# Kernel tuning notes

Measured on AMD Instinct MI355X. Metric: run time of the kernel, lower is better.

## Reference

```python
import jax, jax.numpy as jnp
import numpy as np

EPS = 1e-12  # torch F.normalize default eps
DN = ('NCHW', 'OIHW', 'NCHW')

def _conv(x, w, groups=1):
    return jax.lax.conv_general_dilated(x, w, window_strides=(1, 1), padding='SAME',
                                        feature_group_count=groups, dimension_numbers=DN)

def setup_inputs() -> dict:
    key = jax.random.key(0)
    k1, k2, k3, k4 = jax.random.split(key, 4)
    b, c, h, w = 4, 64, 64, 64
    x = jax.random.normal(k1, (b, c, h, w), dtype=jnp.float32)
    w_qkv = jax.random.normal(k2, (3 * c, c, 1, 1), dtype=jnp.float32) * (1.0 / np.sqrt(c))
    w_dw = jax.random.normal(k3, (3 * c, 1, 3, 3), dtype=jnp.float32) * (1.0 / 3.0)
    w_proj = jax.random.normal(k4, (c, c, 3, 3), dtype=jnp.float32) * (1.0 / np.sqrt(9 * c))
    return {"x": x, "w_qkv": w_qkv, "w_dw": w_dw, "w_proj": w_proj}

def _l2norm(t):
    # torch F.normalize(dim=-1): t / max(||t||_2, eps)
    n = jnp.sqrt(jnp.sum(t * t, axis=-1, keepdims=True))
    return t / jnp.maximum(n, EPS)

def reference(x, w_qkv, w_dw, w_proj):
    b, c, h, w = x.shape
    qkv = _conv(_conv(x, w_qkv), w_dw, groups=3 * c)  # (b, 3c, h, w)
    q, k, v = jnp.split(qkv, 3, axis=1)
    hw = h * w
    q = _l2norm(q.reshape(b, c, hw))  # normalize each channel's spatial vector
    k = _l2norm(k.reshape(b, c, hw))
    v = v.reshape(b, c, hw)
    attn = jnp.einsum('bcn,bcm->bnm', q, k)        # (b, hw, hw) cosine scores
    attn = jax.nn.softmax(attn, axis=-1)
    out = jnp.einsum('bcm,bmn->bcn', v, attn)       # v @ attn
    out = out.reshape(b, c, h, w)
    return _conv(out, w_proj)
```

## Files before the change

### kernel.cpp

```cpp
#include <hip/hip_runtime.h>
#include <hip/hip_bf16.h>

typedef __attribute__((ext_vector_type(8))) short bf16x8;
typedef __attribute__((ext_vector_type(4))) float f32x4;
typedef __attribute__((ext_vector_type(8))) unsigned short ushort8;

#define HW 4096
#define NC 64
#define PROWS 4356

static __device__ __forceinline__ unsigned short f2bf(float f) {
    unsigned int u = __float_as_uint(f);
    unsigned int r = (u + 0x7FFFu + ((u >> 16) & 1u)) >> 16;
    return (unsigned short)r;
}

__global__ __launch_bounds__(256) void k_conv1x1(const float* __restrict__ x,
                                                 const float* __restrict__ wqkv,
                                                 float* __restrict__ out) {
    __shared__ float wl[512];
    int nb = blockIdx.x, ocg = blockIdx.y, b = blockIdx.z;
    int t = threadIdx.x;
    for (int i = t; i < 512; i += 256) wl[i] = wqkv[ocg * 512 + i];
    __syncthreads();
    int n = nb * 256 + t;
    const float* xb = x + (size_t)b * NC * HW + n;
    float acc[8] = {0.f,0.f,0.f,0.f,0.f,0.f,0.f,0.f};
    for (int ic = 0; ic < 64; ic++) {
        float xv = xb[(size_t)ic * HW];
        #pragma unroll
        for (int o = 0; o < 8; o++) acc[o] += wl[o * 64 + ic] * xv;
    }
    float* ob = out + (size_t)b * 192 * HW + (size_t)(ocg * 8) * HW + n;
    #pragma unroll
    for (int o = 0; o < 8; o++) ob[(size_t)o * HW] = acc[o];
}

__global__ __launch_bounds__(256) void k_dwconv(const float* __restrict__ in,
                                                const float* __restrict__ wdw,
                                                float* __restrict__ out) {
    int yg = blockIdx.x, ch = blockIdx.y, b = blockIdx.z;
    int t = threadIdx.x;
    int y = yg * 4 + (t >> 6), xx = t & 63;
    const float* ib = in + ((size_t)b * 192 + ch) * HW;
    const float* wp = wdw + ch * 9;
    float s = 0.f;
    #pragma unroll
    for (int dy = 0; dy < 3; dy++) {
        int yy = y + dy - 1;
        if (yy < 0 || yy > 63) continue;
        const float* r = ib + yy * 64;
        float v0 = (xx > 0) ? r[xx - 1] : 0.f;
        float v1 = r[xx];
        float v2 = (xx < 63) ? r[xx + 1] : 0.f;
        const float* wr = wp + dy * 3;
        s += wr[0] * v0 + wr[1] * v1 + wr[2] * v2;
    }
    out[((size_t)b * 192 + ch) * HW + y * 64 + xx] = s;
}

__global__ __launch_bounds__(256) void k_norms(const float* __restrict__ qkv,
                                               float* __restrict__ invn) {
    int ch = blockIdx.x, b = blockIdx.y;
    const float* p = qkv + ((size_t)b * 192 + ch) * HW;
    float s = 0.f;
    for (int i = threadIdx.x; i < HW; i += 256) { float v = p[i]; s += v * v; }
    #pragma unroll
    for (int m = 1; m < 64; m <<= 1) s += __shfl_xor(s, m);
    __shared__ float red[4];
    if ((threadIdx.x & 63) == 0) red[threadIdx.x >> 6] = s;
    __syncthreads();
    if (threadIdx.x == 0) {
        float tot = red[0] + red[1] + red[2] + red[3];
        float nrm = sqrtf(tot);
        invn[b * 128 + ch] = 1.f / fmaxf(nrm, 1e-12f);
    }
}

__global__ __launch_bounds__(256) void k_pack(const float* __restrict__ qkv,
                                              const float* __restrict__ invn,
                                              unsigned short* __restrict__ qT,
                                              unsigned short* __restrict__ kT,
                                              unsigned short* __restrict__ vn) {
    int nb = blockIdx.x, sel = blockIdx.y, b = blockIdx.z;
    int n = nb * 256 + threadIdx.x;
    if (sel == 2) {
        const float* src = qkv + ((size_t)b * 192 + 128) * HW + n;
        unsigned short* dst = vn + (size_t)b * NC * HW + n;
        for (int c = 0; c < 64; c++) dst[(size_t)c * HW] = f2bf(src[(size_t)c * HW]);
    } else {
        const float* src = qkv + ((size_t)b * 192 + sel * 64) * HW + n;
        const float* iv = invn + b * 128 + sel * 64;
        unsigned short* dst = (sel == 0 ? qT : kT) + ((size_t)b * HW + n) * NC;
        for (int c0 = 0; c0 < 64; c0 += 8) {
            ushort8 pk;
            #pragma unroll
            for (int j = 0; j < 8; j++)
                pk[j] = f2bf(src[(size_t)(c0 + j) * HW] * iv[c0 + j]);
            *reinterpret_cast<ushort8*>(dst + c0) = pk;
        }
    }
}

__global__ __launch_bounds__(256) void k_rowsum(const unsigned short* __restrict__ qT,
                                                const unsigned short* __restrict__ kT,
                                                float* __restrict__ part) {
    __shared__ __align__(16) unsigned short klds[2][64 * 72];
    int mblk = blockIdx.x, ns = blockIdx.y, b = blockIdx.z;
    int t = threadIdx.x;
    int w = t >> 6, lane = t & 63, g = lane >> 4, r15 = lane & 15;
    const unsigned short* qb = qT + (size_t)b * HW * NC;
    const unsigned short* kb = kT + (size_t)b * HW * NC;
    int m0 = mblk * 128 + w * 16;
    const unsigned short* qp0 = qb + (size_t)(m0 + r15) * NC + g * 8;
    const unsigned short* qp1 = qb + (size_t)(m0 + 64 + r15) * NC + g * 8;
    bf16x8 a0 = *reinterpret_cast<const bf16x8*>(qp0);
    bf16x8 a1 = *reinterpret_cast<const bf16x8*>(qp0 + 32);
    bf16x8 a2 = *reinterpret_cast<const bf16x8*>(qp1);
    bf16x8 a3 = *reinterpret_cast<const bf16x8*>(qp1 + 32);
    float sa[4] = {0.f, 0.f, 0.f, 0.f};
    float sb[4] = {0.f, 0.f, 0.f, 0.f};
    int nbase = ns * 512;
    int nl = t >> 2, seg = t & 3;
    {
        const unsigned short* sp = kb + (size_t)(nbase + nl) * NC + seg * 16;
        *reinterpret_cast<ushort8*>(&klds[0][nl * 72 + seg * 16]) = *reinterpret_cast<const ushort8*>(sp);
        *reinterpret_cast<ushort8*>(&klds[0][nl * 72 + seg * 16 + 8]) = *reinterpret_cast<const ushort8*>(sp + 8);
    }
    __syncthreads();
    int cur = 0;
    for (int it = 0; it < 8; it++) {
        ushort8 r0, r1;
        bool hasnext = it < 7;
        if (hasnext) {
            const unsigned short* sp = kb + (size_t)(nbase + (it + 1) * 64 + nl) * NC + seg * 16;
            r0 = *reinterpret_cast<const ushort8*>(sp);
            r1 = *reinterpret_cast<const ushort8*>(sp + 8);
        }
        #pragma unroll
        for (int tt = 0; tt < 4; tt++) {
            const unsigned short* kp = &klds[cur][(tt * 16 + r15) * 72 + g * 8];
            bf16x8 b0 = *reinterpret_cast<const bf16x8*>(kp);
            bf16x8 b1 = *reinterpret_cast<const bf16x8*>(kp + 32);
            f32x4 d0 = {0.f, 0.f, 0.f, 0.f};
            f32x4 d1 = {0.f, 0.f, 0.f, 0.f};
            d0 = __builtin_amdgcn_mfma_f32_16x16x32_bf16(a0, b0, d0, 0, 0, 0);
            d1 = __builtin_amdgcn_mfma_f32_16x16x32_bf16(a2, b0, d1, 0, 0, 0);
            d0 = __builtin_amdgcn_mfma_f32_16x16x32_bf16(a1, b1, d0, 0, 0, 0);
            d1 = __builtin_amdgcn_mfma_f32_16x16x32_bf16(a3, b1, d1, 0, 0, 0);
            #pragma unroll
            for (int r = 0; r < 4; r++) { sa[r] += __expf(d0[r]); sb[r] += __expf(d1[r]); }
        }
        if (hasnext) {
            *reinterpret_cast<ushort8*>(&klds[cur ^ 1][nl * 72 + seg * 16]) = r0;
            *reinterpret_cast<ushort8*>(&klds[cur ^ 1][nl * 72 + seg * 16 + 8]) = r1;
            cur ^= 1;
        }
        __syncthreads();
    }
    #pragma unroll
    for (int off = 1; off < 16; off <<= 1) {
        #pragma unroll
        for (int r = 0; r < 4; r++) {
            sa[r] += __shfl_xor(sa[r], off);
            sb[r] += __shfl_xor(sb[r], off);
        }
    }
    if (r15 == 0) {
        size_t base = ((size_t)ns * 4 + b) * HW;
        f32x4 va = {sa[0], sa[1], sa[2], sa[3]};
        f32x4 vb = {sb[0], sb[1], sb[2], sb[3]};
        *reinterpret_cast<f32x4*>(&part[base + m0 + g * 4]) = va;
        *reinterpret_cast<f32x4*>(&part[base + m0 + 64 + g * 4]) = vb;
    }
}

__global__ __launch_bounds__(256) void k_recip(const float* __restrict__ part,
                                               float* __restrict__ inv) {
    int i = blockIdx.x * 256 + threadIdx.x;
    float s = 0.f;
    #pragma unroll
    for (int ns = 0; ns < 8; ns++) s += part[i + ns * 4 * HW];
    inv[i] = 1.f / s;
}

__global__ __launch_bounds__(512, 2) void k_attn_fused(const unsigned short* __restrict__ qT,
                                                       const unsigned short* __restrict__ kT,
                                                       const unsigned short* __restrict__ vn,
                                                       const float* __restrict__ rowinv,
                                                       unsigned short* __restrict__ inP) {
    __shared__ float red[8][64][8];
    int nb = blockIdx.x, b = blockIdx.y;
    int t = threadIdx.x;
    int w = t >> 6, lane = t & 63, g = lane >> 4, r15 = lane & 15;
    int n0 = nb * 64;
    const unsigned short* qb = qT + (size_t)b * HW * NC;
    const unsigned short* kbp = kT + (size_t)b * HW * NC;
    const unsigned short* vb = vn + (size_t)b * NC * HW;
    const float* rib = rowinv + (size_t)b * HW;
    bf16x8 kf0[4], kf1[4];
    #pragma unroll
    for (int tt = 0; tt < 4; tt++) {
        const unsigned short* kp = kbp + (size_t)(n0 + tt * 16 + r15) * NC + g * 8;
        kf0[tt] = *reinterpret_cast<const bf16x8*>(kp);
        kf1[tt] = *reinterpret_cast<const bf16x8*>(kp + 32);
    }
    f32x4 acc[4][4];
    #pragma unroll
    for (int ct = 0; ct < 4; ct++)
        #pragma unroll
        for (int tt = 0; tt < 4; tt++) acc[ct][tt] = f32x4{0.f, 0.f, 0.f, 0.f};
    int mw = w * 32;
    int qrow = (r15 >> 2) * 8 + (r15 & 3);
    const unsigned short* qrp = qb + (size_t)(mw + qrow) * NC;
    bf16x8 qa[2][2];
    #pragma unroll
    for (int ts = 0; ts < 2; ts++) {
        qa[ts][0] = *reinterpret_cast<const bf16x8*>(qrp + ts * 4 * NC + g * 8);
        qa[ts][1] = *reinterpret_cast<const bf16x8*>(qrp + ts * 4 * NC + 32 + g * 8);
    }
    f32x4 iv[2];
    iv[0] = *reinterpret_cast<const f32x4*>(rib + mw + g * 8);
    iv[1] = *reinterpret_cast<const f32x4*>(rib + mw + g * 8 + 4);
    for (int it = 0; it < 16; it++) {
        int mb = it * 256;
        bf16x8 va[4];
        #pragma unroll
        for (int ct = 0; ct < 4; ct++)
            va[ct] = *reinterpret_cast<const bf16x8*>(vb + (size_t)(ct * 16 + r15) * HW + mb + mw + g * 8);
        int adv = (it < 15) ? 256 : 0;
        const unsigned short* qrn = qrp + (size_t)adv * NC;
        bf16x8 qn[2][2];
        #pragma unroll
        for (int ts = 0; ts < 2; ts++) {
            qn[ts][0] = *reinterpret_cast<const bf16x8*>(qrn + ts * 4 * NC + g * 8);
            qn[ts][1] = *reinterpret_cast<const bf16x8*>(qrn + ts * 4 * NC + 32 + g * 8);
        }
        f32x4 ivn0 = *reinterpret_cast<const f32x4*>(rib + mb + adv + mw + g * 8);
        f32x4 ivn1 = *reinterpret_cast<const f32x4*>(rib + mb + adv + mw + g * 8 + 4);
        bf16x8 pb[4];
        #pragma unroll
        for (int tt = 0; tt < 4; tt++) {
            f32x4 z = {0.f, 0.f, 0.f, 0.f};
            f32x4 d0 = __builtin_amdgcn_mfma_f32_16x16x32_bf16(qa[0][0], kf0[tt], z, 0, 0, 0);
            d0 = __builtin_amdgcn_mfma_f32_16x16x32_bf16(qa[0][1], kf1[tt], d0, 0, 0, 0);
            f32x4 d1 = __builtin_amdgcn_mfma_f32_16x16x32_bf16(qa[1][0], kf0[tt], z, 0, 0, 0);
            d1 = __builtin_amdgcn_mfma_f32_16x16x32_bf16(qa[1][1], kf1[tt], d1, 0, 0, 0);
            float e0 = __expf(d0[0]) * iv[0][0];
            float e1 = __expf(d0[1]) * iv[0][1];
            float e2 = __expf(d0[2]) * iv[0][2];
            float e3 = __expf(d0[3]) * iv[0][3];
            float f0 = __expf(d1[0]) * iv[1][0];
            float f1 = __expf(d1[1]) * iv[1][1];
            float f2 = __expf(d1[2]) * iv[1][2];
            float f3 = __expf(d1[3]) * iv[1][3];
            unsigned int p0, p1, p2, p3;
            asm("v_cvt_pk_bf16_f32 %0, %1, %2" : "=v"(p0) : "v"(e0), "v"(e1));
            asm("v_cvt_pk_bf16_f32 %0, %1, %2" : "=v"(p1) : "v"(e2), "v"(e3));
            asm("v_cvt_pk_bf16_f32 %0, %1, %2" : "=v"(p2) : "v"(f0), "v"(f1));
            asm("v_cvt_pk_bf16_f32 %0, %1, %2" : "=v"(p3) : "v"(f2), "v"(f3));
            union { unsigned int u[4]; bf16x8 v; } pu;
            pu.u[0] = p0; pu.u[1] = p1; pu.u[2] = p2; pu.u[3] = p3;
            pb[tt] = pu.v;
        }
        #pragma unroll
        for (int ct = 0; ct < 4; ct++)
            #pragma unroll
            for (int tt = 0; tt < 4; tt++)
                acc[ct][tt] = __builtin_amdgcn_mfma_f32_16x16x32_bf16(va[ct], pb[tt], acc[ct][tt], 0, 0, 0);
        #pragma unroll
        for (int ts = 0; ts < 2; ts++) { qa[ts][0] = qn[ts][0]; qa[ts][1] = qn[ts][1]; }
        iv[0] = ivn0; iv[1] = ivn1;
        qrp += (size_t)adv * NC;
    }
    #pragma unroll
    for (int ph = 0; ph < 8; ph++) {
        int ct = ph >> 1, th = ph & 1;
        *reinterpret_cast<f32x4*>(&red[w][lane][0]) = acc[ct][th * 2];
        *reinterpret_cast<f32x4*>(&red[w][lane][4]) = acc[ct][th * 2 + 1];
        __syncthreads();
        int lr = t >> 3, kk = t & 7;
        float s = 0.f;
        #pragma unroll
        for (int ww = 0; ww < 8; ww++) s += red[ww][lr][kk];
        int c = ct * 16 + ((lr >> 4) << 2) + (kk & 3);
        int nn = n0 + (th * 2 + (kk >> 2)) * 16 + (lr & 15);
        int y = nn >> 6, xx = nn & 63;
        inP[((size_t)b * PROWS + (size_t)(y + 1) * 66 + 1 + xx) * 64 + c] = f2bf(s);
        __syncthreads();
    }
}

__global__ __launch_bounds__(256) void k_zero(float4* __restrict__ p, int n4) {
    int i = blockIdx.x * 256 + threadIdx.x;
    if (i < n4) p[i] = make_float4(0.f, 0.f, 0.f, 0.f);
}

__global__ __launch_bounds__(256) void k_wconv(const float* __restrict__ wp,
                                               unsigned short* __restrict__ wbf) {
    int idx = blockIdx.x * 256 + threadIdx.x;
    int tap = idx >> 12;
    int rem = idx & 4095;
    int oc = rem >> 6, ic = rem & 63;
    wbf[idx] = f2bf(wp[(oc * 64 + ic) * 9 + tap]);
}

__global__ __launch_bounds__(256) void k_proj_mfma(const unsigned short* __restrict__ inP,
                                                   const unsigned short* __restrict__ wbf,
                                                   float* __restrict__ out) {
    int nb = blockIdx.x, b = blockIdx.y;
    int t = threadIdx.x;
    int w = t >> 6, lane = t & 63, g = lane >> 4, r15 = lane & 15;
    int y = nb >> 1;
    int x0 = (nb & 1) * 32 + (w & 1) * 16;
    int oc0 = (w >> 1) * 32;
    const unsigned short* base = inP + (size_t)b * PROWS * 64;
    f32x4 acc[2] = {{0.f,0.f,0.f,0.f},{0.f,0.f,0.f,0.f}};
    #pragma unroll
    for (int tap = 0; tap < 9; tap++) {
        int dy = tap / 3, dx = tap % 3;
        int p = (y + dy) * 66 + x0 + dx + r15;
        const unsigned short* bp = base + (size_t)p * 64 + g * 8;
        bf16x8 b0 = *reinterpret_cast<const bf16x8*>(bp);
        bf16x8 b1 = *reinterpret_cast<const bf16x8*>(bp + 32);
        #pragma unroll
        for (int tt = 0; tt < 2; tt++) {
            const unsigned short* ap = wbf + tap * 4096 + (size_t)(oc0 + tt * 16 + r15) * 64 + g * 8;
            bf16x8 a0 = *reinterpret_cast<const bf16x8*>(ap);
            bf16x8 a1 = *reinterpret_cast<const bf16x8*>(ap + 32);
            acc[tt] = __builtin_amdgcn_mfma_f32_16x16x32_bf16(a0, b0, acc[tt], 0, 0, 0);
            acc[tt] = __builtin_amdgcn_mfma_f32_16x16x32_bf16(a1, b1, acc[tt], 0, 0, 0);
        }
    }
    int n0 = y * 64 + x0;
    #pragma unroll
    for (int tt = 0; tt < 2; tt++) {
        #pragma unroll
        for (int r = 0; r < 4; r++)
            out[((size_t)b * 64 + oc0 + tt * 16 + g * 4 + r) * HW + n0 + r15] = acc[tt][r];
    }
}

extern "C" void kernel_launch(void* const* d_in, const int* in_sizes, int n_in,
                              void* d_out, int out_size, void* d_ws, size_t ws_size,
                              hipStream_t stream) {
    const float* x    = (const float*)d_in[0];
    const float* wqkv = (const float*)d_in[1];
    const float* wdw  = (const float*)d_in[2];
    const float* wprj = (const float*)d_in[3];
    char* ws = (char*)d_ws;
    float* qkv_raw       = (float*)(ws + 0);
    float* qkv           = (float*)(ws + 12582912);
    unsigned short* qT   = (unsigned short*)(ws + 25165824);
    unsigned short* kT   = (unsigned short*)(ws + 27262976);
    unsigned short* vn   = (unsigned short*)(ws + 29360128);
    float* invn          = (float*)(ws + 31457280);
    float* rowsum_part   = (float*)(ws + 31459328);
    float* rowinv        = (float*)(ws + 31983616);
    unsigned short* wbf  = (unsigned short*)(ws + 32049152);
    unsigned short* inP  = (unsigned short*)(ws + 32122880);

    int inP4 = (4 * PROWS * 64 * 2) / 16;
    k_zero       <<<dim3((inP4 + 255) / 256), 256, 0, stream>>>((float4*)inP, inP4);
    k_wconv      <<<dim3(144),        256, 0, stream>>>(wprj, wbf);
    k_conv1x1    <<<dim3(16, 24, 4),  256, 0, stream>>>(x, wqkv, qkv_raw);
    k_dwconv     <<<dim3(16, 192, 4), 256, 0, stream>>>(qkv_raw, wdw, qkv);
    k_norms      <<<dim3(128, 4),     256, 0, stream>>>(qkv, invn);
    k_pack       <<<dim3(16, 3, 4),   256, 0, stream>>>(qkv, invn, qT, kT, vn);
    k_rowsum     <<<dim3(32, 8, 4),   256, 0, stream>>>(qT, kT, rowsum_part);
    k_recip      <<<dim3(64),         256, 0, stream>>>(rowsum_part, rowinv);
    k_attn_fused <<<dim3(64, 4),      512, 0, stream>>>(qT, kT, vn, rowinv, inP);
    k_proj_mfma  <<<dim3(128, 4),     256, 0, stream>>>(inP, wbf, (float*)d_out);
}
```

Baseline: 115.8 us.

## Fuse norms into dwconv, fold softmax scaling into exp2 and halve attention tile

The depthwise conv now emits partial sums of squares, and a tiny kernel folds both q and k inverse norms plus log2(e) into a single per-channel scale applied to k. This removes the separate norm reduction pass. The row-sum reciprocal becomes -log2(sum), which is injected as the MFMA accumulator init, so exp2 directly yields normalized probabilities and the per-element multiply disappears. The attention kernel's column tile is halved to 32 with launch bounds of 4 waves per SIMD, doubling the grid for occupancy. The cost is that each block reloads the q fragments without software prefetch, and bf16 rounding now applies to the combined scale.

Measured after the change: 146.4 us. 1.26x slower.

```diff
diff --git a/kernel.cpp b/kernel.cpp
--- a/kernel.cpp
+++ b/kernel.cpp
@@ -38,7 +38,8 @@
 
 __global__ __launch_bounds__(256) void k_dwconv(const float* __restrict__ in,
                                                 const float* __restrict__ wdw,
-                                                float* __restrict__ out) {
+                                                float* __restrict__ out,
+                                                float* __restrict__ psq) {
     int yg = blockIdx.x, ch = blockIdx.y, b = blockIdx.z;
     int t = threadIdx.x;
     int y = yg * 4 + (t >> 6), xx = t & 63;
@@ -57,28 +58,34 @@
         s += wr[0] * v0 + wr[1] * v1 + wr[2] * v2;
     }
     out[((size_t)b * 192 + ch) * HW + y * 64 + xx] = s;
-}
-
-__global__ __launch_bounds__(256) void k_norms(const float* __restrict__ qkv,
-                                               float* __restrict__ invn) {
-    int ch = blockIdx.x, b = blockIdx.y;
-    const float* p = qkv + ((size_t)b * 192 + ch) * HW;
-    float s = 0.f;
-    for (int i = threadIdx.x; i < HW; i += 256) { float v = p[i]; s += v * v; }
-    #pragma unroll
-    for (int m = 1; m < 64; m <<= 1) s += __shfl_xor(s, m);
-    __shared__ float red[4];
-    if ((threadIdx.x & 63) == 0) red[threadIdx.x >> 6] = s;
-    __syncthreads();
-    if (threadIdx.x == 0) {
-        float tot = red[0] + red[1] + red[2] + red[3];
-        float nrm = sqrtf(tot);
-        invn[b * 128 + ch] = 1.f / fmaxf(nrm, 1e-12f);
-    }
+    if (ch < 128) {
+        float sq = s * s;
+        #pragma unroll
+        for (int m = 1; m < 64; m <<= 1) sq += __shfl_xor(sq, m);
+        __shared__ float red[4];
+        if ((t & 63) == 0) red[t >> 6] = sq;
+        __syncthreads();
+        if (t == 0)
+            psq[((size_t)b * 128 + ch) * 16 + yg] = red[0] + red[1] + red[2] + red[3];
+    }
+}
+
+__global__ __launch_bounds__(256) void k_scales(const float* __restrict__ psq,
+                                                float* __restrict__ wk) {
+    int i = threadIdx.x;
+    int b = i >> 6, c = i & 63;
+    const float* pq = psq + ((size_t)b * 128 + c) * 16;
+    const float* pk = psq + ((size_t)b * 128 + 64 + c) * 16;
+    float sq = 0.f, sk = 0.f;
+    #pragma unroll
+    for (int j = 0; j < 16; j++) { sq += pq[j]; sk += pk[j]; }
+    float nq = fmaxf(sqrtf(sq), 1e-12f);
+    float nk = fmaxf(sqrtf(sk), 1e-12f);
+    wk[i] = 1.4426950408889634f / (nq * nk);
 }
 
 __global__ __launch_bounds__(256) void k_pack(const float* __restrict__ qkv,
-                                              const float* __restrict__ invn,
+                                              const float* __restrict__ wk,
                                               unsigned short* __restrict__ qT,
                                               unsigned short* __restrict__ kT,
                                               unsigned short* __restrict__ vn) {
@@ -88,15 +95,24 @@
         const float* src = qkv + ((size_t)b * 192 + 128) * HW + n;
         unsigned short* dst = vn + (size_t)b * NC * HW + n;
         for (int c = 0; c < 64; c++) dst[(size_t)c * HW] = f2bf(src[(size_t)c * HW]);
+    } else if (sel == 0) {
+        const float* src = qkv + (size_t)b * 192 * HW + n;
+        unsigned short* dst = qT + ((size_t)b * HW + n) * NC;
+        for (int c0 = 0; c0 < 64; c0 += 8) {
+            ushort8 pk;
+            #pragma unroll
+            for (int j = 0; j < 8; j++) pk[j] = f2bf(src[(size_t)(c0 + j) * HW]);
+            *reinterpret_cast<ushort8*>(dst + c0) = pk;
+        }
     } else {
-        const float* src = qkv + ((size_t)b * 192 + sel * 64) * HW + n;
-        const float* iv = invn + b * 128 + sel * 64;
-        unsigned short* dst = (sel == 0 ? qT : kT) + ((size_t)b * HW + n) * NC;
+        const float* src = qkv + ((size_t)b * 192 + 64) * HW + n;
+        const float* wv = wk + b * 64;
+        unsigned short* dst = kT + ((size_t)b * HW + n) * NC;
         for (int c0 = 0; c0 < 64; c0 += 8) {
             ushort8 pk;
             #pragma unroll
             for (int j = 0; j < 8; j++)
-                pk[j] = f2bf(src[(size_t)(c0 + j) * HW] * iv[c0 + j]);
+                pk[j] = f2bf(src[(size_t)(c0 + j) * HW] * wv[c0 + j]);
             *reinterpret_cast<ushort8*>(dst + c0) = pk;
         }
     }
@@ -149,7 +165,7 @@
             d0 = __builtin_amdgcn_mfma_f32_16x16x32_bf16(a1, b1, d0, 0, 0, 0);
             d1 = __builtin_amdgcn_mfma_f32_16x16x32_bf16(a3, b1, d1, 0, 0, 0);
             #pragma unroll
-            for (int r = 0; r < 4; r++) { sa[r] += __expf(d0[r]); sb[r] += __expf(d1[r]); }
+            for (int r = 0; r < 4; r++) { sa[r] += exp2f(d0[r]); sb[r] += exp2f(d1[r]); }
         }
         if (hasnext) {
             *reinterpret_cast<ushort8*>(&klds[cur ^ 1][nl * 72 + seg * 16]) = r0;
@@ -175,85 +191,71 @@
     }
 }
 
-__global__ __launch_bounds__(256) void k_recip(const float* __restrict__ part,
-                                               float* __restrict__ inv) {
+__global__ __launch_bounds__(256) void k_l2i(const float* __restrict__ part,
+                                             float* __restrict__ l2i) {
     int i = blockIdx.x * 256 + threadIdx.x;
     float s = 0.f;
     #pragma unroll
     for (int ns = 0; ns < 8; ns++) s += part[i + ns * 4 * HW];
-    inv[i] = 1.f / s;
-}
-
-__global__ __launch_bounds__(512, 2) void k_attn_fused(const unsigned short* __restrict__ qT,
+    l2i[i] = -log2f(s);
+}
+
+__global__ __launch_bounds__(512, 4) void k_attn_fused(const unsigned short* __restrict__ qT,
                                                        const unsigned short* __restrict__ kT,
                                                        const unsigned short* __restrict__ vn,
-                                                       const float* __restrict__ rowinv,
+                                                       const float* __restrict__ l2i,
                                                        unsigned short* __restrict__ inP) {
     __shared__ float red[8][64][8];
     int nb = blockIdx.x, b = blockIdx.y;
     int t = threadIdx.x;
     int w = t >> 6, lane = t & 63, g = lane >> 4, r15 = lane & 15;
-    int n0 = nb * 64;
+    int n0 = nb * 32;
     const unsigned short* qb = qT + (size_t)b * HW * NC;
     const unsigned short* kbp = kT + (size_t)b * HW * NC;
     const unsigned short* vb = vn + (size_t)b * NC * HW;
-    const float* rib = rowinv + (size_t)b * HW;
-    bf16x8 kf0[4], kf1[4];
-    #pragma unroll
-    for (int tt = 0; tt < 4; tt++) {
+    const float* rib = l2i + (size_t)b * HW;
+    bf16x8 kf0[2], kf1[2];
+    #pragma unroll
+    for (int tt = 0; tt < 2; tt++) {
         const unsigned short* kp = kbp + (size_t)(n0 + tt * 16 + r15) * NC + g * 8;
         kf0[tt] = *reinterpret_cast<const bf16x8*>(kp);
         kf1[tt] = *reinterpret_cast<const bf16x8*>(kp + 32);
     }
-    f32x4 acc[4][4];
+    f32x4 acc[4][2];
     #pragma unroll
     for (int ct = 0; ct < 4; ct++)
         #pragma unroll
-        for (int tt = 0; tt < 4; tt++) acc[ct][tt] = f32x4{0.f, 0.f, 0.f, 0.f};
+        for (int tt = 0; tt < 2; tt++) acc[ct][tt] = f32x4{0.f, 0.f, 0.f, 0.f};
     int mw = w * 32;
     int qrow = (r15 >> 2) * 8 + (r15 & 3);
-    const unsigned short* qrp = qb + (size_t)(mw + qrow) * NC;
-    bf16x8 qa[2][2];
-    #pragma unroll
-    for (int ts = 0; ts < 2; ts++) {
-        qa[ts][0] = *reinterpret_cast<const bf16x8*>(qrp + ts * 4 * NC + g * 8);
-        qa[ts][1] = *reinterpret_cast<const bf16x8*>(qrp + ts * 4 * NC + 32 + g * 8);
-    }
-    f32x4 iv[2];
-    iv[0] = *reinterpret_cast<const f32x4*>(rib + mw + g * 8);
-    iv[1] = *reinterpret_cast<const f32x4*>(rib + mw + g * 8 + 4);
     for (int it = 0; it < 16; it++) {
         int mb = it * 256;
+        const unsigned short* qrp = qb + (size_t)(mb + mw + qrow) * NC;
+        bf16x8 qa00 = *reinterpret_cast<const bf16x8*>(qrp + g * 8);
+        bf16x8 qa01 = *reinterpret_cast<const bf16x8*>(qrp + 32 + g * 8);
+        bf16x8 qa10 = *reinterpret_cast<const bf16x8*>(qrp + 4 * NC + g * 8);
+        bf16x8 qa11 = *reinterpret_cast<const bf16x8*>(qrp + 4 * NC + 32 + g * 8);
+        f32x4 iv0 = *reinterpret_cast<const f32x4*>(rib + mb + mw + g * 8);
+        f32x4 iv1 = *reinterpret_cast<const f32x4*>(rib + mb + mw + g * 8 + 4);
         bf16x8 va[4];
         #pragma unroll
         for (int ct = 0; ct < 4; ct++)
             va[ct] = *reinterpret_cast<const bf16x8*>(vb + (size_t)(ct * 16 + r15) * HW + mb + mw + g * 8);
-        int adv = (it < 15) ? 256 : 0;
-        const unsigned short* qrn = qrp + (size_t)adv * NC;
-        bf16x8 qn[2][2];
-        #pragma unroll
-        for (int ts = 0; ts < 2; ts++) {
-            qn[ts][0] = *reinterpret_cast<const bf16x8*>(qrn + ts * 4 * NC + g * 8);
-            qn[ts][1] = *reinterpret_cast<const bf16x8*>(qrn + ts * 4 * NC + 32 + g * 8);
-        }
-        f32x4 ivn0 = *reinterpret_cast<const f32x4*>(rib + mb + adv + mw + g * 8);
-        f32x4 ivn1 = *reinterpret_cast<const f32x4*>(rib + mb + adv + mw + g * 8 + 4);
-        bf16x8 pb[4];
-        #pragma unroll
-        for (int tt = 0; tt < 4; tt++) {
-            f32x4 z = {0.f, 0.f, 0.f, 0.f};
-            f32x4 d0 = __builtin_amdgcn_mfma_f32_16x16x32_bf16(qa[0][0], kf0[tt], z, 0, 0, 0);
-            d0 = __builtin_amdgcn_mfma_f32_16x16x32_bf16(qa[0][1], kf1[tt], d0, 0, 0, 0);
-            f32x4 d1 = __builtin_amdgcn_mfma_f32_16x16x32_bf16(qa[1][0], kf0[tt], z, 0, 0, 0);
-            d1 = __builtin_amdgcn_mfma_f32_16x16x32_bf16(qa[1][1], kf1[tt], d1, 0, 0, 0);
-            float e0 = __expf(d0[0]) * iv[0][0];
-            float e1 = __expf(d0[1]) * iv[0][1];
-            float e2 = __expf(d0[2]) * iv[0][2];
-            float e3 = __expf(d0[3]) * iv[0][3];
-            float f0 = __expf(d1[0]) * iv[1][0];
-            float f1 = __expf(d1[1]) * iv[1][1];
-            float f2 = __expf(d1[2]) * iv[1][2];
-            float f3 = __expf(d1[3]) * iv[1][3];
+        bf16x8 pb[2];
+        #pragma unroll
+        for (int tt = 0; tt < 2; tt++) {
+            f32x4 d0 = __builtin_amdgcn_mfma_f32_16x16x32_bf16(qa00, kf0[tt], iv0, 0, 0, 0);
+            d0 = __builtin_amdgcn_mfma_f32_16x16x32_bf16(qa01, kf1[tt], d0, 0, 0, 0);
+            f32x4 d1 = __builtin_amdgcn_mfma_f32_16x16x32_bf16(qa10, kf0[tt], iv1, 0, 0, 0);
+            d1 = __builtin_amdgcn_mfma_f32_16x16x32_bf16(qa11, kf1[tt], d1, 0, 0, 0);
+            float e0 = exp2f(d0[0]);
+            float e1 = exp2f(d0[1]);
+            float e2 = exp2f(d0[2]);
+            float e3 = exp2f(d0[3]);
+            float f0 = exp2f(d1[0]);
+            float f1 = exp2f(d1[1]);
+            float f2 = exp2f(d1[2]);
+            float f3 = exp2f(d1[3]);
             unsigned int p0, p1, p2, p3;
             asm("v_cvt_pk_bf16_f32 %0, %1, %2" : "=v"(p0) : "v"(e0), "v"(e1));
             asm("v_cvt_pk_bf16_f32 %0, %1, %2" : "=v"(p1) : "v"(e2), "v"(e3));
@@ -266,25 +268,20 @@
         #pragma unroll
         for (int ct = 0; ct < 4; ct++)
             #pragma unroll
-            for (int tt = 0; tt < 4; tt++)
+            for (int tt = 0; tt < 2; tt++)
                 acc[ct][tt] = __builtin_amdgcn_mfma_f32_16x16x32_bf16(va[ct], pb[tt], acc[ct][tt], 0, 0, 0);
-        #pragma unroll
-        for (int ts = 0; ts < 2; ts++) { qa[ts][0] = qn[ts][0]; qa[ts][1] = qn[ts][1]; }
-        iv[0] = ivn0; iv[1] = ivn1;
-        qrp += (size_t)adv * NC;
-    }
-    #pragma unroll
-    for (int ph = 0; ph < 8; ph++) {
-        int ct = ph >> 1, th = ph & 1;
-        *reinterpret_cast<f32x4*>(&red[w][lane][0]) = acc[ct][th * 2];
-        *reinterpret_cast<f32x4*>(&red[w][lane][4]) = acc[ct][th * 2 + 1];
+    }
+    #pragma unroll
+    for (int ph = 0; ph < 4; ph++) {
+        *reinterpret_cast<f32x4*>(&red[w][lane][0]) = acc[ph][0];
+        *reinterpret_cast<f32x4*>(&red[w][lane][4]) = acc[ph][1];
         __syncthreads();
         int lr = t >> 3, kk = t & 7;
         float s = 0.f;
         #pragma unroll
         for (int ww = 0; ww < 8; ww++) s += red[ww][lr][kk];
-        int c = ct * 16 + ((lr >> 4) << 2) + (kk & 3);
-        int nn = n0 + (th * 2 + (kk >> 2)) * 16 + (lr & 15);
+        int c = ph * 16 + ((lr >> 4) << 2) + (kk & 3);
+        int nn = n0 + (kk >> 2) * 16 + (lr & 15);
         int y = nn >> 6, xx = nn & 63;
         inP[((size_t)b * PROWS + (size_t)(y + 1) * 66 + 1 + xx) * 64 + c] = f2bf(s);
         __syncthreads();
@@ -354,21 +351,22 @@
     unsigned short* qT   = (unsigned short*)(ws + 25165824);
     unsigned short* kT   = (unsigned short*)(ws + 27262976);
     unsigned short* vn   = (unsigned short*)(ws + 29360128);
-    float* invn          = (float*)(ws + 31457280);
-    float* rowsum_part   = (float*)(ws + 31459328);
-    float* rowinv        = (float*)(ws + 31983616);
-    unsigned short* wbf  = (unsigned short*)(ws + 32049152);
-    unsigned short* inP  = (unsigned short*)(ws + 32122880);
+    float* psq           = (float*)(ws + 31457280);
+    float* wk            = (float*)(ws + 31490048);
+    float* rowsum_part   = (float*)(ws + 31491072);
+    float* l2i           = (float*)(ws + 32015360);
+    unsigned short* wbf  = (unsigned short*)(ws + 32080896);
+    unsigned short* inP  = (unsigned short*)(ws + 32154624);
 
     int inP4 = (4 * PROWS * 64 * 2) / 16;
     k_zero       <<<dim3((inP4 + 255) / 256), 256, 0, stream>>>((float4*)inP, inP4);
     k_wconv      <<<dim3(144),        256, 0, stream>>>(wprj, wbf);
     k_conv1x1    <<<dim3(16, 24, 4),  256, 0, stream>>>(x, wqkv, qkv_raw);
-    k_dwconv     <<<dim3(16, 192, 4), 256, 0, stream>>>(qkv_raw, wdw, qkv);
-    k_norms      <<<dim3(128, 4),     256, 0, stream>>>(qkv, invn);
-    k_pack       <<<dim3(16, 3, 4),   256, 0, stream>>>(qkv, invn, qT, kT, vn);
+    k_dwconv     <<<dim3(16, 192, 4), 256, 0, stream>>>(qkv_raw, wdw, qkv, psq);
+    k_scales     <<<dim3(1),          256, 0, stream>>>(psq, wk);
+    k_pack       <<<dim3(16, 3, 4),   256, 0, stream>>>(qkv, wk, qT, kT, vn);
     k_rowsum     <<<dim3(32, 8, 4),   256, 0, stream>>>(qT, kT, rowsum_part);
-    k_recip      <<<dim3(64),         256, 0, stream>>>(rowsum_part, rowinv);
-    k_attn_fused <<<dim3(64, 4),      512, 0, stream>>>(qT, kT, vn, rowinv, inP);
+    k_l2i        <<<dim3(64),         256, 0, stream>>>(rowsum_part, l2i);
+    k_attn_fused <<<dim3(128, 4),     512, 0, stream>>>(qT, kT, vn, l2i, inP);
     k_proj_mfma  <<<dim3(128, 4),     256, 0, stream>>>(inP, wbf, (float*)d_out);
 }
```
